# Performance work log

Measured on AMD Instinct MI355X. Metric: run time of the kernel, lower is better.

The kernel has to match this reference:

```python
import jax, jax.numpy as jnp
import numpy as np

B, N, FEAT_DIM = 64, 4096, 256
N_SLOTS, SLOT_DIM, N_ITERS = 6, 64, 3
EPS_LN = 1e-5

def _ln(x, g, b):
    m = jnp.mean(x, axis=-1, keepdims=True)
    v = jnp.mean((x - m) ** 2, axis=-1, keepdims=True)
    return (x - m) * jax.lax.rsqrt(v + EPS_LN) * g + b

def setup_inputs() -> dict:
    key = jax.random.key(0)
    ks = jax.random.split(key, 16)
    def lin(k, out_d, in_d):  # torch Linear default init scale
        bound = 1.0 / np.sqrt(in_d)
        return jax.random.uniform(k, (out_d, in_d), jnp.float32, -bound, bound)
    H = SLOT_DIM
    bound_h = 1.0 / np.sqrt(H)
    return {
        "features": jax.random.normal(ks[0], (B, N, FEAT_DIM), jnp.float32),
        "slot_noise": jax.random.normal(ks[1], (B, N_SLOTS, SLOT_DIM), jnp.float32),
        "slot_mu": jax.random.normal(ks[2], (1, 1, SLOT_DIM), jnp.float32) * 0.02,
        "slot_sigma": jnp.ones((1, 1, SLOT_DIM), jnp.float32) * 0.1,
        "ln_feat_g": jnp.ones((FEAT_DIM,), jnp.float32),
        "ln_feat_b": jnp.zeros((FEAT_DIM,), jnp.float32),
        "ln_slot_g": jnp.ones((SLOT_DIM,), jnp.float32),
        "ln_slot_b": jnp.zeros((SLOT_DIM,), jnp.float32),
        "ln_mlp_g": jnp.ones((SLOT_DIM,), jnp.float32),
        "ln_mlp_b": jnp.zeros((SLOT_DIM,), jnp.float32),
        "Wk": lin(ks[3], SLOT_DIM, FEAT_DIM),
        "Wv": lin(ks[4], SLOT_DIM, FEAT_DIM),
        "Wq": lin(ks[5], SLOT_DIM, SLOT_DIM),
        "W_ih": jax.random.uniform(ks[6], (3 * H, H), jnp.float32, -bound_h, bound_h),
        "W_hh": jax.random.uniform(ks[7], (3 * H, H), jnp.float32, -bound_h, bound_h),
        "b_ih": jax.random.uniform(ks[8], (3 * H,), jnp.float32, -bound_h, bound_h),
        "b_hh": jax.random.uniform(ks[9], (3 * H,), jnp.float32, -bound_h, bound_h),
        "mlp_W1": lin(ks[10], 2 * SLOT_DIM, SLOT_DIM),
        "mlp_b1": jnp.zeros((2 * SLOT_DIM,), jnp.float32),
        "mlp_W2": lin(ks[11], SLOT_DIM, 2 * SLOT_DIM),
        "mlp_b2": jnp.zeros((SLOT_DIM,), jnp.float32),
    }

def _gru(x, h, W_ih, W_hh, b_ih, b_hh):
    # torch.nn.GRUCell semantics; x, h: [M, H]
    gi = x @ W_ih.T + b_ih
    gh = h @ W_hh.T + b_hh
    i_r, i_z, i_n = jnp.split(gi, 3, axis=-1)
    h_r, h_z, h_n = jnp.split(gh, 3, axis=-1)
    r = jax.nn.sigmoid(i_r + h_r)
    z = jax.nn.sigmoid(i_z + h_z)
    n = jnp.tanh(i_n + r * h_n)
    return (1.0 - z) * n + z * h

def reference(features, slot_noise, slot_mu, slot_sigma,
              ln_feat_g, ln_feat_b, ln_slot_g, ln_slot_b, ln_mlp_g, ln_mlp_b,
              Wk, Wv, Wq, W_ih, W_hh, b_ih, b_hh,
              mlp_W1, mlp_b1, mlp_W2, mlp_b2):
    slots = slot_mu + slot_sigma * slot_noise            # [B, K, H]
    f = _ln(features, ln_feat_g, ln_feat_b)              # [B, N, D]
    k = jnp.einsum('bnd,hd->bnh', f, Wk)                 # [B, N, H]
    v = jnp.einsum('bnd,hd->bnh', f, Wv)                 # [B, N, H]
    scale = SLOT_DIM ** (-0.5)
    for _ in range(N_ITERS):
        slots_prev = slots
        s = _ln(slots, ln_slot_g, ln_slot_b)
        q = jnp.einsum('bkh,gh->bkg', s, Wq)             # [B, K, H]
        attn = jnp.einsum('bkh,bnh->bkn', q, k) * scale  # [B, K, N]
        attn = jax.nn.softmax(attn, axis=1)              # softmax over SLOT dim
        attn = attn / (jnp.sum(attn, axis=-1, keepdims=True) + 1e-8)
        updates = jnp.einsum('bkn,bnh->bkh', attn, v)    # [B, K, H]
        h = _gru(updates.reshape(-1, SLOT_DIM), slots_prev.reshape(-1, SLOT_DIM),
                 W_ih, W_hh, b_ih, b_hh)
        slots = h.reshape(B, N_SLOTS, SLOT_DIM)
        m = _ln(slots, ln_mlp_g, ln_mlp_b)
        m = jax.nn.relu(m @ mlp_W1.T + mlp_b1) @ mlp_W2.T + mlp_b2
        slots = slots + m
    return slots
```

## Files before the change

kernel.cpp:

```cpp
#include <hip/hip_runtime.h>
#include <hip/hip_bf16.h>
#include <math.h>

#define B_SZ    64
#define N_TOK   4096
#define D_FEAT  256
#define K_SLOTS 6
#define H_DIM   64
#define N_IT    3
#define CHUNKS  8
#define LNKV_BLOCKS 512
#define TILES_PER_BLOCK 8

typedef __attribute__((ext_vector_type(8))) __bf16 bf16x8;
typedef __attribute__((ext_vector_type(4))) __bf16 bf16x4;
typedef __attribute__((ext_vector_type(4))) float  f32x4v;

__device__ __forceinline__ float wave_reduce_sum(float v) {
    #pragma unroll
    for (int off = 32; off > 0; off >>= 1) v += __shfl_xor(v, off, 64);
    return v;
}
__device__ __forceinline__ float bflo(unsigned u) { return __builtin_bit_cast(float, (unsigned)(u << 16)); }
__device__ __forceinline__ float bfhi(unsigned u) { return __builtin_bit_cast(float, (unsigned)(u & 0xffff0000u)); }

__global__ __launch_bounds__(256) void prep_kernel(
    const float* __restrict__ Wk, const float* __restrict__ Wv,
    const float* __restrict__ noise, const float* __restrict__ mu,
    const float* __restrict__ sigma, const float* __restrict__ Wq,
    const float* __restrict__ W_ih, const float* __restrict__ W_hh,
    const float* __restrict__ W1, const float* __restrict__ W2,
    __bf16* __restrict__ Wfrag, float* __restrict__ slots,
    float* __restrict__ WqT, float* __restrict__ WihT, float* __restrict__ WhhT,
    float* __restrict__ W1T, float* __restrict__ W2T)
{
    const int tg = blockIdx.x * 256 + threadIdx.x;
    if (tg < 4096) {
        const int chunk = tg >> 6, lane = tg & 63;
        const int ct = chunk >> 3, ks = chunk & 7;
        const int outr = ct * 16 + (lane & 15);
        const int dbase = (lane >> 4) * 8 + ks * 32;
        const float* srcw = (outr < 64) ? &Wk[outr * 256] : &Wv[(outr - 64) * 256];
        bf16x8 w8;
        #pragma unroll
        for (int j = 0; j < 8; ++j) w8[j] = (__bf16)srcw[dbase + j];
        *(bf16x8*)&Wfrag[(size_t)tg * 8] = w8;
    } else if (tg < 4096 + 24576) {
        const int i = tg - 4096;
        const int hh = i & 63;
        slots[i] = mu[hh] + sigma[hh] * noise[i];
    } else if (tg < 32768) {
        const int i = tg - 28672;
        WqT[i] = Wq[(i & 63) * 64 + (i >> 6)];
    } else if (tg < 45056) {
        const int i = tg - 32768;
        WihT[i] = W_ih[(i % 192) * 64 + (i / 192)];
    } else if (tg < 57344) {
        const int i = tg - 45056;
        WhhT[i] = W_hh[(i % 192) * 64 + (i / 192)];
    } else if (tg < 65536) {
        const int i = tg - 57344;
        W1T[i] = W1[(i & 127) * 64 + (i >> 7)];
    } else if (tg < 73728) {
        const int i = tg - 65536;
        W2T[i] = W2[(i & 63) * 128 + (i >> 6)];
    }
}

__global__ __launch_bounds__(256, 1) void ln_kv_mfma(
    const float* __restrict__ feat, const float* __restrict__ g,
    const float* __restrict__ bta, const __bf16* __restrict__ Wfrag,
    __bf16* __restrict__ kv)
{
    __shared__ __align__(16) __bf16 W_lds[32768];
    __shared__ __align__(16) __bf16 A_lds[64][264];
    __shared__ __align__(16) __bf16 C_lds[64][136];

    const int t = threadIdx.x;
    const int lane = t & 63;
    const int w = t >> 6;
    const int m15 = lane & 15;
    const int q4 = lane >> 4;

    {
        const uint4* src = (const uint4*)Wfrag;
        uint4* dst = (uint4*)W_lds;
        #pragma unroll
        for (int i = 0; i < 16; ++i) dst[i * 256 + t] = src[i * 256 + t];
    }
    __syncthreads();

    const float4 gg = *(const float4*)&g[lane * 4];
    const float4 bb = *(const float4*)&bta[lane * 4];

    float4 x[16];
    {
        const size_t row0 = (size_t)blockIdx.x * TILES_PER_BLOCK * 64 + w * 16;
        #pragma unroll
        for (int r = 0; r < 16; ++r)
            x[r] = *(const float4*)&feat[(row0 + r) * D_FEAT + lane * 4];
    }

    for (int tile = 0; tile < TILES_PER_BLOCK; ++tile) {
        const size_t tile_row0 = (size_t)blockIdx.x * TILES_PER_BLOCK * 64 + (size_t)tile * 64;

        #pragma unroll
        for (int r = 0; r < 16; ++r) {
            float s1 = x[r].x + x[r].y + x[r].z + x[r].w;
            float s2 = x[r].x * x[r].x + x[r].y * x[r].y + x[r].z * x[r].z + x[r].w * x[r].w;
            s1 = wave_reduce_sum(s1);
            s2 = wave_reduce_sum(s2);
            const float m = s1 * (1.0f / 256.0f);
            const float inv = rsqrtf(s2 * (1.0f / 256.0f) - m * m + 1e-5f);
            bf16x4 y;
            y[0] = (__bf16)((x[r].x - m) * inv * gg.x + bb.x);
            y[1] = (__bf16)((x[r].y - m) * inv * gg.y + bb.y);
            y[2] = (__bf16)((x[r].z - m) * inv * gg.z + bb.z);
            y[3] = (__bf16)((x[r].w - m) * inv * gg.w + bb.w);
            *(bf16x4*)&A_lds[w * 16 + r][lane * 4] = y;
        }

        if (tile + 1 < TILES_PER_BLOCK) {
            const size_t row0 = tile_row0 + 64 + w * 16;
            #pragma unroll
            for (int r = 0; r < 16; ++r)
                x[r] = *(const float4*)&feat[(row0 + r) * D_FEAT + lane * 4];
        }

        bf16x8 af[8];
        #pragma unroll
        for (int ks = 0; ks < 8; ++ks)
            af[ks] = *(const bf16x8*)&A_lds[w * 16 + m15][q4 * 8 + ks * 32];

        f32x4v acc[8];
        #pragma unroll
        for (int ct = 0; ct < 8; ++ct) acc[ct] = (f32x4v){0.f, 0.f, 0.f, 0.f};

        #pragma unroll
        for (int ks = 0; ks < 8; ++ks) {
            #pragma unroll
            for (int ct = 0; ct < 8; ++ct) {
                const bf16x8 bfr = *(const bf16x8*)&W_lds[((ct * 8 + ks) * 64 + lane) * 8];
                acc[ct] = __builtin_amdgcn_mfma_f32_16x16x32_bf16(af[ks], bfr, acc[ct], 0, 0, 0);
            }
        }

        #pragma unroll
        for (int ct = 0; ct < 8; ++ct) {
            #pragma unroll
            for (int reg = 0; reg < 4; ++reg)
                C_lds[w * 16 + q4 * 4 + reg][ct * 16 + m15] = (__bf16)acc[ct][reg];
        }
        const int lr = w * 16 + (lane >> 2);
        const int seg = lane & 3;
        __bf16* dstg = kv + (tile_row0 + lr) * 128 + seg * 32;
        #pragma unroll
        for (int u = 0; u < 4; ++u) {
            const uint4 val = *(const uint4*)&C_lds[lr][seg * 32 + u * 8];
            *(uint4*)&dstg[u * 8] = val;
        }
    }
}

__global__ __launch_bounds__(64) void slot_q0(
    const float* __restrict__ slots, const float* __restrict__ g,
    const float* __restrict__ bta, const float* __restrict__ WqT,
    float* __restrict__ qb)
{
    __shared__ float s_lds[64];
    const int bk = blockIdx.x, h = threadIdx.x;
    const float xv = slots[bk * 64 + h];
    const float s1 = wave_reduce_sum(xv);
    const float s2 = wave_reduce_sum(xv * xv);
    const float m = s1 * (1.0f / 64.0f);
    const float inv = rsqrtf(s2 * (1.0f / 64.0f) - m * m + 1e-5f);
    s_lds[h] = (xv - m) * inv * g[h] + bta[h];
    __syncthreads();
    float acc = 0.f;
    #pragma unroll 8
    for (int j = 0; j < 64; ++j) acc += WqT[j * 64 + h] * s_lds[j];
    qb[bk * 64 + h] = acc;
}

__global__ __launch_bounds__(256) void attn_kernel(
    const float* __restrict__ qb, const __bf16* __restrict__ kv,
    float* __restrict__ U_part, float* __restrict__ S_part)
{
    __shared__ float q_lds[K_SLOTS * 64];
    __shared__ __align__(16) float KVt[64][130];
    __shared__ float p_lds[K_SLOTS][64];
    __shared__ float U_red[4][K_SLOTS][64];
    __shared__ float S_red[4][K_SLOTS];

    const int t = threadIdx.x;
    const int b = blockIdx.y;
    const int chunk = blockIdx.x;
    const int lane = t & 63;
    const int w = t >> 6;
    const int n_loc = t >> 2, sub = t & 3;
    const int h = lane;

    for (int i = t; i < K_SLOTS * 64; i += 256) q_lds[i] = qb[b * K_SLOTS * 64 + i];

    float Uacc[K_SLOTS] = {0, 0, 0, 0, 0, 0};
    float Sacc[K_SLOTS] = {0, 0, 0, 0, 0, 0};

    for (int tile = 0; tile < 8; ++tile) {
        __syncthreads();
        const size_t n0 = (size_t)b * N_TOK + (size_t)chunk * (N_TOK / CHUNKS) + tile * 64;
        {
            const uint4* src = (const uint4*)&kv[(n0 + lane) * 128 + w * 32];
            float2* drow = (float2*)&KVt[lane][w * 32];
            #pragma unroll
            for (int u = 0; u < 4; ++u) {
                const uint4 pk = src[u];
                drow[u * 4 + 0] = make_float2(bflo(pk.x), bfhi(pk.x));
                drow[u * 4 + 1] = make_float2(bflo(pk.y), bfhi(pk.y));
                drow[u * 4 + 2] = make_float2(bflo(pk.z), bfhi(pk.z));
                drow[u * 4 + 3] = make_float2(bflo(pk.w), bfhi(pk.w));
            }
        }
        __syncthreads();

        float part[K_SLOTS] = {0, 0, 0, 0, 0, 0};
        #pragma unroll
        for (int i = 0; i < 16; ++i) {
            const float kvv = KVt[n_loc][sub * 16 + i];
            #pragma unroll
            for (int k = 0; k < K_SLOTS; ++k) part[k] += q_lds[k * 64 + sub * 16 + i] * kvv;
        }
        #pragma unroll
        for (int k = 0; k < K_SLOTS; ++k) {
            part[k] += __shfl_xor(part[k], 1, 64);
            part[k] += __shfl_xor(part[k], 2, 64);
        }
        float mx = part[0];
        #pragma unroll
        for (int k = 1; k < K_SLOTS; ++k) mx = fmaxf(mx, part[k]);
        float e[K_SLOTS], ssum = 0.f;
        #pragma unroll
        for (int k = 0; k < K_SLOTS; ++k) { e[k] = __expf((part[k] - mx) * 0.125f); ssum += e[k]; }
        mx = part[0] * 0.125f;
        #pragma unroll
        for (int k = 1; k < K_SLOTS; ++k) mx = fmaxf(mx, part[k] * 0.125f);
        ssum = 0.f;
        #pragma unroll
        for (int k = 0; k < K_SLOTS; ++k) { e[k] = __expf(part[k] * 0.125f - mx); ssum += e[k]; }
        const float rs = 1.0f / ssum;
        if (sub == 0) {
            #pragma unroll
            for (int k = 0; k < K_SLOTS; ++k) {
                const float p = e[k] * rs;
                p_lds[k][n_loc] = p;
                Sacc[k] += p;
            }
        }
        __syncthreads();

        for (int n = w * 16; n < w * 16 + 16; ++n) {
            const float vv = KVt[n][64 + h];
            #pragma unroll
            for (int k = 0; k < K_SLOTS; ++k) Uacc[k] += p_lds[k][n] * vv;
        }
    }

    #pragma unroll
    for (int k = 0; k < K_SLOTS; ++k) U_red[w][k][h] = Uacc[k];
    #pragma unroll
    for (int k = 0; k < K_SLOTS; ++k) {
        const float s = wave_reduce_sum(Sacc[k]);
        if (lane == 0) S_red[w][k] = s;
    }
    __syncthreads();
    for (int idx = t; idx < K_SLOTS * 64; idx += 256) {
        const int k = idx >> 6, hh = idx & 63;
        const float s = U_red[0][k][hh] + U_red[1][k][hh] + U_red[2][k][hh] + U_red[3][k][hh];
        U_part[(((size_t)b * CHUNKS + chunk) * K_SLOTS + k) * 64 + hh] = s;
    }
    if (t < K_SLOTS) {
        const float s = S_red[0][t] + S_red[1][t] + S_red[2][t] + S_red[3][t];
        S_part[((size_t)b * CHUNKS + chunk) * K_SLOTS + t] = s;
    }
}

__global__ __launch_bounds__(64) void update_kernel(
    const float* __restrict__ U_part, const float* __restrict__ S_part,
    float* __restrict__ slots,
    const float* __restrict__ WihT, const float* __restrict__ WhhT,
    const float* __restrict__ b_ih, const float* __restrict__ b_hh,
    const float* __restrict__ g_mlp, const float* __restrict__ b_mlp,
    const float* __restrict__ W1T, const float* __restrict__ b1,
    const float* __restrict__ W2T, const float* __restrict__ b2,
    const float* __restrict__ g_slot, const float* __restrict__ b_slot,
    const float* __restrict__ WqT, float* __restrict__ qb,
    float* __restrict__ out, int last)
{
    __shared__ float x_lds[64], h_lds[64], m_lds[64], r_lds[128];
    const int bk = blockIdx.x, h = threadIdx.x;
    const int b = bk / K_SLOTS, k = bk % K_SLOTS;

    float Us = 0.f, Ss = 0.f;
    #pragma unroll
    for (int c = 0; c < CHUNKS; ++c)
        Us += U_part[(((size_t)b * CHUNKS + c) * K_SLOTS + k) * 64 + h];
    #pragma unroll
    for (int c = 0; c < CHUNKS; ++c)
        Ss += S_part[((size_t)b * CHUNKS + c) * K_SLOTS + k];

    const float u = Us / (Ss + 1e-8f);
    const float hp = slots[bk * 64 + h];
    x_lds[h] = u;
    h_lds[h] = hp;
    __syncthreads();

    float ir = b_ih[h], iz = b_ih[64 + h], inn = b_ih[128 + h];
    float hr = b_hh[h], hz = b_hh[64 + h], hn = b_hh[128 + h];
    #pragma unroll 4
    for (int j = 0; j < 64; ++j) {
        const float xj = x_lds[j], hj = h_lds[j];
        const float* wi = &WihT[j * 192];
        const float* wh = &WhhT[j * 192];
        ir += wi[h] * xj; iz += wi[64 + h] * xj; inn += wi[128 + h] * xj;
        hr += wh[h] * hj; hz += wh[64 + h] * hj; hn += wh[128 + h] * hj;
    }
    const float r = 1.0f / (1.0f + __expf(-(ir + hr)));
    const float z = 1.0f / (1.0f + __expf(-(iz + hz)));
    const float nn = tanhf(inn + r * hn);
    const float hnew = (1.0f - z) * nn + z * hp;

    const float s1 = wave_reduce_sum(hnew);
    const float s2 = wave_reduce_sum(hnew * hnew);
    const float m = s1 * (1.0f / 64.0f);
    const float inv = rsqrtf(s2 * (1.0f / 64.0f) - m * m + 1e-5f);
    m_lds[h] = (hnew - m) * inv * g_mlp[h] + b_mlp[h];
    __syncthreads();

    float a1 = b1[h], a2 = b1[64 + h];
    #pragma unroll 4
    for (int j = 0; j < 64; ++j) {
        const float mj = m_lds[j];
        a1 += W1T[j * 128 + h] * mj;
        a2 += W1T[j * 128 + 64 + h] * mj;
    }
    r_lds[h] = fmaxf(a1, 0.f);
    r_lds[64 + h] = fmaxf(a2, 0.f);
    __syncthreads();

    float o = b2[h];
    #pragma unroll 4
    for (int c = 0; c < 128; ++c) o += W2T[c * 64 + h] * r_lds[c];

    const float res = hnew + o;
    slots[bk * 64 + h] = res;
    if (last) {
        out[bk * 64 + h] = res;
    } else {
        const float t1 = wave_reduce_sum(res);
        const float t2 = wave_reduce_sum(res * res);
        const float mm = t1 * (1.0f / 64.0f);
        const float ii = rsqrtf(t2 * (1.0f / 64.0f) - mm * mm + 1e-5f);
        m_lds[h] = (res - mm) * ii * g_slot[h] + b_slot[h];
        __syncthreads();
        float qv = 0.f;
        #pragma unroll 8
        for (int j = 0; j < 64; ++j) qv += WqT[j * 64 + h] * m_lds[j];
        qb[bk * 64 + h] = qv;
    }
}

extern "C" void kernel_launch(void* const* d_in, const int* in_sizes, int n_in,
                              void* d_out, int out_size, void* d_ws, size_t ws_size,
                              hipStream_t stream) {
    const float* feat      = (const float*)d_in[0];
    const float* noise     = (const float*)d_in[1];
    const float* mu        = (const float*)d_in[2];
    const float* sigma     = (const float*)d_in[3];
    const float* ln_feat_g = (const float*)d_in[4];
    const float* ln_feat_b = (const float*)d_in[5];
    const float* ln_slot_g = (const float*)d_in[6];
    const float* ln_slot_b = (const float*)d_in[7];
    const float* ln_mlp_g  = (const float*)d_in[8];
    const float* ln_mlp_b  = (const float*)d_in[9];
    const float* Wk        = (const float*)d_in[10];
    const float* Wv        = (const float*)d_in[11];
    const float* Wq        = (const float*)d_in[12];
    const float* W_ih      = (const float*)d_in[13];
    const float* W_hh      = (const float*)d_in[14];
    const float* b_ih      = (const float*)d_in[15];
    const float* b_hh      = (const float*)d_in[16];
    const float* W1        = (const float*)d_in[17];
    const float* b1        = (const float*)d_in[18];
    const float* W2        = (const float*)d_in[19];
    const float* b2        = (const float*)d_in[20];
    float* out = (float*)d_out;

    char* p = (char*)d_ws;
    __bf16* kv    = (__bf16*)p;                 p += (size_t)B_SZ * N_TOK * 128 * 2;
    __bf16* Wfrag = (__bf16*)p;                 p += 32768 * 2;
    float* slots  = (float*)p;                  p += 24576 * 4;
    float* qb     = (float*)p;                  p += 24576 * 4;
    float* U_part = (float*)p;                  p += (size_t)B_SZ * CHUNKS * K_SLOTS * 64 * 4;
    float* S_part = (float*)p;                  p += (size_t)B_SZ * CHUNKS * K_SLOTS * 4;
    float* WqT    = (float*)p;                  p += 4096 * 4;
    float* WihT   = (float*)p;                  p += 12288 * 4;
    float* WhhT   = (float*)p;                  p += 12288 * 4;
    float* W1T    = (float*)p;                  p += 8192 * 4;
    float* W2T    = (float*)p;                  p += 8192 * 4;

    hipLaunchKernelGGL(prep_kernel, dim3(288), dim3(256), 0, stream,
                       Wk, Wv, noise, mu, sigma, Wq, W_ih, W_hh, W1, W2,
                       Wfrag, slots, WqT, WihT, WhhT, W1T, W2T);
    hipLaunchKernelGGL(ln_kv_mfma, dim3(LNKV_BLOCKS), dim3(256), 0, stream,
                       feat, ln_feat_g, ln_feat_b, Wfrag, kv);
    hipLaunchKernelGGL(slot_q0, dim3(384), dim3(64), 0, stream,
                       slots, ln_slot_g, ln_slot_b, WqT, qb);
    for (int it = 0; it < N_IT; ++it) {
        hipLaunchKernelGGL(attn_kernel, dim3(CHUNKS, B_SZ), dim3(256), 0, stream,
                           qb, kv, U_part, S_part);
        hipLaunchKernelGGL(update_kernel, dim3(384), dim3(64), 0, stream,
                           U_part, S_part, slots, WihT, WhhT, b_ih, b_hh,
                           ln_mlp_g, ln_mlp_b, W1T, b1, W2T, b2,
                           ln_slot_g, ln_slot_b, WqT, qb,
                           out, (it == N_IT - 1) ? 1 : 0);
    }
}
```

Before: 575.3 us.

## Fuse all slot iterations into one per-batch kernel with MFMA attention

Replaces the per-iteration attention and update kernel pairs with a single kernel that runs one 1024-thread block per batch. That block computes slot init, q projection, attention with MFMA, GRU and MLP for all three iterations. The LN/KV projection kernel now uses 512-thread blocks and writes K row-major and V transposed so V can be fed directly as MFMA operands. The aim is to remove kernel launches, partial-sum round trips through global memory and fp32 LDS conversion. The cost is that only 64 blocks run the iteration phase, which limits parallelism over a 4096-token sweep per iteration.

```diff
diff --git a/kernel.cpp b/kernel.cpp
--- a/kernel.cpp
+++ b/kernel.cpp
@@ -8,9 +8,8 @@
 #define K_SLOTS 6
 #define H_DIM   64
 #define N_IT    3
-#define CHUNKS  8
-#define LNKV_BLOCKS 512
-#define TILES_PER_BLOCK 8
+#define LNKV_BLOCKS 256
+#define LNKV_TILES  8
 
 typedef __attribute__((ext_vector_type(8))) __bf16 bf16x8;
 typedef __attribute__((ext_vector_type(4))) __bf16 bf16x4;
@@ -21,17 +20,14 @@
     for (int off = 32; off > 0; off >>= 1) v += __shfl_xor(v, off, 64);
     return v;
 }
-__device__ __forceinline__ float bflo(unsigned u) { return __builtin_bit_cast(float, (unsigned)(u << 16)); }
-__device__ __forceinline__ float bfhi(unsigned u) { return __builtin_bit_cast(float, (unsigned)(u & 0xffff0000u)); }
 
 __global__ __launch_bounds__(256) void prep_kernel(
     const float* __restrict__ Wk, const float* __restrict__ Wv,
-    const float* __restrict__ noise, const float* __restrict__ mu,
-    const float* __restrict__ sigma, const float* __restrict__ Wq,
-    const float* __restrict__ W_ih, const float* __restrict__ W_hh,
-    const float* __restrict__ W1, const float* __restrict__ W2,
-    __bf16* __restrict__ Wfrag, float* __restrict__ slots,
-    float* __restrict__ WqT, float* __restrict__ WihT, float* __restrict__ WhhT,
+    const float* __restrict__ Wq, const float* __restrict__ W_ih,
+    const float* __restrict__ W_hh, const float* __restrict__ W1,
+    const float* __restrict__ W2,
+    __bf16* __restrict__ Wfrag, float* __restrict__ WqT,
+    float* __restrict__ WihT, float* __restrict__ WhhT,
     float* __restrict__ W1T, float* __restrict__ W2T)
 {
     const int tg = blockIdx.x * 256 + threadIdx.x;
@@ -45,64 +41,56 @@
         #pragma unroll
         for (int j = 0; j < 8; ++j) w8[j] = (__bf16)srcw[dbase + j];
         *(bf16x8*)&Wfrag[(size_t)tg * 8] = w8;
-    } else if (tg < 4096 + 24576) {
-        const int i = tg - 4096;
-        const int hh = i & 63;
-        slots[i] = mu[hh] + sigma[hh] * noise[i];
+    } else if (tg < 8192) {
+        const int i = tg - 4096;  WqT[i] = Wq[(i & 63) * 64 + (i >> 6)];
+    } else if (tg < 20480) {
+        const int i = tg - 8192;  WihT[i] = W_ih[(i % 192) * 64 + (i / 192)];
     } else if (tg < 32768) {
-        const int i = tg - 28672;
-        WqT[i] = Wq[(i & 63) * 64 + (i >> 6)];
-    } else if (tg < 45056) {
-        const int i = tg - 32768;
-        WihT[i] = W_ih[(i % 192) * 64 + (i / 192)];
-    } else if (tg < 57344) {
-        const int i = tg - 45056;
-        WhhT[i] = W_hh[(i % 192) * 64 + (i / 192)];
-    } else if (tg < 65536) {
-        const int i = tg - 57344;
-        W1T[i] = W1[(i & 127) * 64 + (i >> 7)];
-    } else if (tg < 73728) {
-        const int i = tg - 65536;
-        W2T[i] = W2[(i & 63) * 128 + (i >> 6)];
+        const int i = tg - 20480; WhhT[i] = W_hh[(i % 192) * 64 + (i / 192)];
+    } else if (tg < 40960) {
+        const int i = tg - 32768; W1T[i] = W1[(i & 127) * 64 + (i >> 7)];
+    } else if (tg < 49152) {
+        const int i = tg - 40960; W2T[i] = W2[(i & 63) * 128 + (i >> 6)];
     }
 }
 
-__global__ __launch_bounds__(256, 1) void ln_kv_mfma(
+__global__ __launch_bounds__(512, 2) void ln_kv_mfma(
     const float* __restrict__ feat, const float* __restrict__ g,
     const float* __restrict__ bta, const __bf16* __restrict__ Wfrag,
-    __bf16* __restrict__ kv)
+    __bf16* __restrict__ kbuf, __bf16* __restrict__ vT)
 {
     __shared__ __align__(16) __bf16 W_lds[32768];
-    __shared__ __align__(16) __bf16 A_lds[64][264];
-    __shared__ __align__(16) __bf16 C_lds[64][136];
+    __shared__ __align__(16) __bf16 S_A[8][16 * 272];
 
     const int t = threadIdx.x;
     const int lane = t & 63;
     const int w = t >> 6;
-    const int m15 = lane & 15;
-    const int q4 = lane >> 4;
+    const int m15 = lane & 15, q4 = lane >> 4;
 
     {
         const uint4* src = (const uint4*)Wfrag;
         uint4* dst = (uint4*)W_lds;
         #pragma unroll
-        for (int i = 0; i < 16; ++i) dst[i * 256 + t] = src[i * 256 + t];
+        for (int i = 0; i < 8; ++i) dst[i * 512 + t] = src[i * 512 + t];
     }
     __syncthreads();
 
     const float4 gg = *(const float4*)&g[lane * 4];
     const float4 bb = *(const float4*)&bta[lane * 4];
 
+    const size_t block_row0 = (size_t)blockIdx.x * (LNKV_TILES * 128);
+    const int b  = blockIdx.x >> 2;
+    const int nq = (blockIdx.x & 3) * 1024;
+
+    __bf16* Aw = &S_A[w][0];
+
     float4 x[16];
-    {
-        const size_t row0 = (size_t)blockIdx.x * TILES_PER_BLOCK * 64 + w * 16;
-        #pragma unroll
-        for (int r = 0; r < 16; ++r)
-            x[r] = *(const float4*)&feat[(row0 + r) * D_FEAT + lane * 4];
-    }
-
-    for (int tile = 0; tile < TILES_PER_BLOCK; ++tile) {
-        const size_t tile_row0 = (size_t)blockIdx.x * TILES_PER_BLOCK * 64 + (size_t)tile * 64;
+    #pragma unroll
+    for (int r = 0; r < 16; ++r)
+        x[r] = *(const float4*)&feat[(block_row0 + w * 16 + r) * D_FEAT + lane * 4];
+
+    for (int tile = 0; tile < LNKV_TILES; ++tile) {
+        const size_t trow0 = block_row0 + (size_t)tile * 128;
 
         #pragma unroll
         for (int r = 0; r < 16; ++r) {
@@ -110,32 +98,30 @@
             float s2 = x[r].x * x[r].x + x[r].y * x[r].y + x[r].z * x[r].z + x[r].w * x[r].w;
             s1 = wave_reduce_sum(s1);
             s2 = wave_reduce_sum(s2);
-            const float m = s1 * (1.0f / 256.0f);
-            const float inv = rsqrtf(s2 * (1.0f / 256.0f) - m * m + 1e-5f);
+            const float m = s1 * (1.f / 256.f);
+            const float inv = rsqrtf(s2 * (1.f / 256.f) - m * m + 1e-5f);
             bf16x4 y;
             y[0] = (__bf16)((x[r].x - m) * inv * gg.x + bb.x);
             y[1] = (__bf16)((x[r].y - m) * inv * gg.y + bb.y);
             y[2] = (__bf16)((x[r].z - m) * inv * gg.z + bb.z);
             y[3] = (__bf16)((x[r].w - m) * inv * gg.w + bb.w);
-            *(bf16x4*)&A_lds[w * 16 + r][lane * 4] = y;
-        }
-
-        if (tile + 1 < TILES_PER_BLOCK) {
-            const size_t row0 = tile_row0 + 64 + w * 16;
+            *(bf16x4*)&Aw[r * 272 + lane * 4] = y;
+        }
+
+        if (tile + 1 < LNKV_TILES) {
             #pragma unroll
             for (int r = 0; r < 16; ++r)
-                x[r] = *(const float4*)&feat[(row0 + r) * D_FEAT + lane * 4];
+                x[r] = *(const float4*)&feat[(trow0 + 128 + w * 16 + r) * D_FEAT + lane * 4];
         }
 
         bf16x8 af[8];
         #pragma unroll
         for (int ks = 0; ks < 8; ++ks)
-            af[ks] = *(const bf16x8*)&A_lds[w * 16 + m15][q4 * 8 + ks * 32];
+            af[ks] = *(const bf16x8*)&Aw[m15 * 272 + q4 * 8 + ks * 32];
 
         f32x4v acc[8];
         #pragma unroll
         for (int ct = 0; ct < 8; ++ct) acc[ct] = (f32x4v){0.f, 0.f, 0.f, 0.f};
-
         #pragma unroll
         for (int ks = 0; ks < 8; ++ks) {
             #pragma unroll
@@ -149,222 +135,233 @@
         for (int ct = 0; ct < 8; ++ct) {
             #pragma unroll
             for (int reg = 0; reg < 4; ++reg)
-                C_lds[w * 16 + q4 * 4 + reg][ct * 16 + m15] = (__bf16)acc[ct][reg];
-        }
-        const int lr = w * 16 + (lane >> 2);
-        const int seg = lane & 3;
-        __bf16* dstg = kv + (tile_row0 + lr) * 128 + seg * 32;
-        #pragma unroll
-        for (int u = 0; u < 4; ++u) {
-            const uint4 val = *(const uint4*)&C_lds[lr][seg * 32 + u * 8];
-            *(uint4*)&dstg[u * 8] = val;
+                Aw[(q4 * 4 + reg) * 136 + ct * 16 + m15] = (__bf16)acc[ct][reg];
+        }
+
+        {
+            const int r = lane >> 2, seg = lane & 3;
+            const bf16x8 k0 = *(const bf16x8*)&Aw[r * 136 + seg * 16];
+            const bf16x8 k1 = *(const bf16x8*)&Aw[r * 136 + seg * 16 + 8];
+            __bf16* kd = kbuf + (trow0 + w * 16 + r) * 64 + seg * 16;
+            *(bf16x8*)&kd[0] = k0;
+            *(bf16x8*)&kd[8] = k1;
+        }
+        {
+            bf16x8 v0, v1;
+            #pragma unroll
+            for (int i = 0; i < 8; ++i) v0[i] = Aw[i * 136 + 64 + lane];
+            #pragma unroll
+            for (int i = 0; i < 8; ++i) v1[i] = Aw[(8 + i) * 136 + 64 + lane];
+            __bf16* vd = vT + ((size_t)b * 64 + lane) * N_TOK + nq + tile * 128 + w * 16;
+            *(bf16x8*)&vd[0] = v0;
+            *(bf16x8*)&vd[8] = v1;
         }
     }
 }
 
-__global__ __launch_bounds__(64) void slot_q0(
-    const float* __restrict__ slots, const float* __restrict__ g,
-    const float* __restrict__ bta, const float* __restrict__ WqT,
-    float* __restrict__ qb)
+__global__ __launch_bounds__(1024, 4) void iters_kernel(
+    const __bf16* __restrict__ kbuf, const __bf16* __restrict__ vT,
+    const float* __restrict__ noise, const float* __restrict__ mu,
+    const float* __restrict__ sigma,
+    const float* __restrict__ g_slot, const float* __restrict__ b_slot,
+    const float* __restrict__ g_mlp, const float* __restrict__ b_mlp,
+    const float* __restrict__ WqT,
+    const float* __restrict__ WihT, const float* __restrict__ WhhT,
+    const float* __restrict__ b_ih, const float* __restrict__ b_hh,
+    const float* __restrict__ W1T, const float* __restrict__ b1,
+    const float* __restrict__ W2T, const float* __restrict__ b2,
+    float* __restrict__ out)
 {
-    __shared__ float s_lds[64];
-    const int bk = blockIdx.x, h = threadIdx.x;
-    const float xv = slots[bk * 64 + h];
-    const float s1 = wave_reduce_sum(xv);
-    const float s2 = wave_reduce_sum(xv * xv);
-    const float m = s1 * (1.0f / 64.0f);
-    const float inv = rsqrtf(s2 * (1.0f / 64.0f) - m * m + 1e-5f);
-    s_lds[h] = (xv - m) * inv * g[h] + bta[h];
-    __syncthreads();
-    float acc = 0.f;
-    #pragma unroll 8
-    for (int j = 0; j < 64; ++j) acc += WqT[j * 64 + h] * s_lds[j];
-    qb[bk * 64 + h] = acc;
-}
-
-__global__ __launch_bounds__(256) void attn_kernel(
-    const float* __restrict__ qb, const __bf16* __restrict__ kv,
-    float* __restrict__ U_part, float* __restrict__ S_part)
-{
-    __shared__ float q_lds[K_SLOTS * 64];
-    __shared__ __align__(16) float KVt[64][130];
-    __shared__ float p_lds[K_SLOTS][64];
-    __shared__ float U_red[4][K_SLOTS][64];
-    __shared__ float S_red[4][K_SLOTS];
-
-    const int t = threadIdx.x;
-    const int b = blockIdx.y;
-    const int chunk = blockIdx.x;
-    const int lane = t & 63;
-    const int w = t >> 6;
-    const int n_loc = t >> 2, sub = t & 3;
-    const int h = lane;
-
-    for (int i = t; i < K_SLOTS * 64; i += 256) q_lds[i] = qb[b * K_SLOTS * 64 + i];
-
-    float Uacc[K_SLOTS] = {0, 0, 0, 0, 0, 0};
-    float Sacc[K_SLOTS] = {0, 0, 0, 0, 0, 0};
-
-    for (int tile = 0; tile < 8; ++tile) {
-        __syncthreads();
-        const size_t n0 = (size_t)b * N_TOK + (size_t)chunk * (N_TOK / CHUNKS) + tile * 64;
-        {
-            const uint4* src = (const uint4*)&kv[(n0 + lane) * 128 + w * 32];
-            float2* drow = (float2*)&KVt[lane][w * 32];
-            #pragma unroll
-            for (int u = 0; u < 4; ++u) {
-                const uint4 pk = src[u];
-                drow[u * 4 + 0] = make_float2(bflo(pk.x), bfhi(pk.x));
-                drow[u * 4 + 1] = make_float2(bflo(pk.y), bfhi(pk.y));
-                drow[u * 4 + 2] = make_float2(bflo(pk.z), bfhi(pk.z));
-                drow[u * 4 + 3] = make_float2(bflo(pk.w), bfhi(pk.w));
-            }
-        }
-        __syncthreads();
-
-        float part[K_SLOTS] = {0, 0, 0, 0, 0, 0};
-        #pragma unroll
-        for (int i = 0; i < 16; ++i) {
-            const float kvv = KVt[n_loc][sub * 16 + i];
-            #pragma unroll
-            for (int k = 0; k < K_SLOTS; ++k) part[k] += q_lds[k * 64 + sub * 16 + i] * kvv;
-        }
-        #pragma unroll
-        for (int k = 0; k < K_SLOTS; ++k) {
-            part[k] += __shfl_xor(part[k], 1, 64);
-            part[k] += __shfl_xor(part[k], 2, 64);
-        }
-        float mx = part[0];
-        #pragma unroll
-        for (int k = 1; k < K_SLOTS; ++k) mx = fmaxf(mx, part[k]);
-        float e[K_SLOTS], ssum = 0.f;
-        #pragma unroll
-        for (int k = 0; k < K_SLOTS; ++k) { e[k] = __expf((part[k] - mx) * 0.125f); ssum += e[k]; }
-        mx = part[0] * 0.125f;
-        #pragma unroll
-        for (int k = 1; k < K_SLOTS; ++k) mx = fmaxf(mx, part[k] * 0.125f);
-        ssum = 0.f;
-        #pragma unroll
-        for (int k = 0; k < K_SLOTS; ++k) { e[k] = __expf(part[k] * 0.125f - mx); ssum += e[k]; }
-        const float rs = 1.0f / ssum;
-        if (sub == 0) {
-            #pragma unroll
-            for (int k = 0; k < K_SLOTS; ++k) {
-                const float p = e[k] * rs;
-                p_lds[k][n_loc] = p;
-                Sacc[k] += p;
-            }
-        }
-        __syncthreads();
-
-        for (int n = w * 16; n < w * 16 + 16; ++n) {
-            const float vv = KVt[n][64 + h];
-            #pragma unroll
-            for (int k = 0; k < K_SLOTS; ++k) Uacc[k] += p_lds[k][n] * vv;
-        }
-    }
-
-    #pragma unroll
-    for (int k = 0; k < K_SLOTS; ++k) U_red[w][k][h] = Uacc[k];
-    #pragma unroll
-    for (int k = 0; k < K_SLOTS; ++k) {
-        const float s = wave_reduce_sum(Sacc[k]);
-        if (lane == 0) S_red[w][k] = s;
+    __shared__ float q_lds[16][64];
+    __shared__ __align__(16) __bf16 p_lds[16][8 * 264];
+    __shared__ float U_red[16][6][64];
+    __shared__ float S_red[16][6][16];
+    __shared__ float slots_lds[6][64], x_lds[6][64], m_lds[6][64], s_lds[6][64];
+    __shared__ float gi_lds[1152], gh_lds[1152];
+    __shared__ float r_lds[6][128];
+    __shared__ float S2[6][16];
+
+    const int t = threadIdx.x, lane = t & 63, w = t >> 6;
+    const int m15 = lane & 15, q4 = lane >> 4;
+    const int b = blockIdx.x;
+    const int kk = t >> 6, hh = t & 63;
+
+    for (int i = lane; i < 528; i += 64) p_lds[w][6 * 264 + i] = (__bf16)0.f;
+    if (t >= 384) { const int i = t - 384; q_lds[6 + (i >> 6)][i & 63] = 0.f; }
+
+    if (t < 384) {
+        const float sv = mu[hh] + sigma[hh] * noise[(b * K_SLOTS + kk) * 64 + hh];
+        slots_lds[kk][hh] = sv;
+        const float s1 = wave_reduce_sum(sv), s2 = wave_reduce_sum(sv * sv);
+        const float m = s1 * (1.f / 64.f);
+        const float inv = rsqrtf(s2 * (1.f / 64.f) - m * m + 1e-5f);
+        s_lds[kk][hh] = (sv - m) * inv * g_slot[hh] + b_slot[hh];
+        float qv = 0.f;
+        #pragma unroll 8
+        for (int j = 0; j < 64; ++j) qv += WqT[j * 64 + hh] * s_lds[kk][j];
+        q_lds[kk][hh] = qv;
     }
     __syncthreads();
-    for (int idx = t; idx < K_SLOTS * 64; idx += 256) {
-        const int k = idx >> 6, hh = idx & 63;
-        const float s = U_red[0][k][hh] + U_red[1][k][hh] + U_red[2][k][hh] + U_red[3][k][hh];
-        U_part[(((size_t)b * CHUNKS + chunk) * K_SLOTS + k) * 64 + hh] = s;
-    }
-    if (t < K_SLOTS) {
-        const float s = S_red[0][t] + S_red[1][t] + S_red[2][t] + S_red[3][t];
-        S_part[((size_t)b * CHUNKS + chunk) * K_SLOTS + t] = s;
-    }
-}
-
-__global__ __launch_bounds__(64) void update_kernel(
-    const float* __restrict__ U_part, const float* __restrict__ S_part,
-    float* __restrict__ slots,
-    const float* __restrict__ WihT, const float* __restrict__ WhhT,
-    const float* __restrict__ b_ih, const float* __restrict__ b_hh,
-    const float* __restrict__ g_mlp, const float* __restrict__ b_mlp,
-    const float* __restrict__ W1T, const float* __restrict__ b1,
-    const float* __restrict__ W2T, const float* __restrict__ b2,
-    const float* __restrict__ g_slot, const float* __restrict__ b_slot,
-    const float* __restrict__ WqT, float* __restrict__ qb,
-    float* __restrict__ out, int last)
-{
-    __shared__ float x_lds[64], h_lds[64], m_lds[64], r_lds[128];
-    const int bk = blockIdx.x, h = threadIdx.x;
-    const int b = bk / K_SLOTS, k = bk % K_SLOTS;
-
-    float Us = 0.f, Ss = 0.f;
-    #pragma unroll
-    for (int c = 0; c < CHUNKS; ++c)
-        Us += U_part[(((size_t)b * CHUNKS + c) * K_SLOTS + k) * 64 + h];
-    #pragma unroll
-    for (int c = 0; c < CHUNKS; ++c)
-        Ss += S_part[((size_t)b * CHUNKS + c) * K_SLOTS + k];
-
-    const float u = Us / (Ss + 1e-8f);
-    const float hp = slots[bk * 64 + h];
-    x_lds[h] = u;
-    h_lds[h] = hp;
-    __syncthreads();
-
-    float ir = b_ih[h], iz = b_ih[64 + h], inn = b_ih[128 + h];
-    float hr = b_hh[h], hz = b_hh[64 + h], hn = b_hh[128 + h];
-    #pragma unroll 4
-    for (int j = 0; j < 64; ++j) {
-        const float xj = x_lds[j], hj = h_lds[j];
-        const float* wi = &WihT[j * 192];
-        const float* wh = &WhhT[j * 192];
-        ir += wi[h] * xj; iz += wi[64 + h] * xj; inn += wi[128 + h] * xj;
-        hr += wh[h] * hj; hz += wh[64 + h] * hj; hn += wh[128 + h] * hj;
-    }
-    const float r = 1.0f / (1.0f + __expf(-(ir + hr)));
-    const float z = 1.0f / (1.0f + __expf(-(iz + hz)));
-    const float nn = tanhf(inn + r * hn);
-    const float hnew = (1.0f - z) * nn + z * hp;
-
-    const float s1 = wave_reduce_sum(hnew);
-    const float s2 = wave_reduce_sum(hnew * hnew);
-    const float m = s1 * (1.0f / 64.0f);
-    const float inv = rsqrtf(s2 * (1.0f / 64.0f) - m * m + 1e-5f);
-    m_lds[h] = (hnew - m) * inv * g_mlp[h] + b_mlp[h];
-    __syncthreads();
-
-    float a1 = b1[h], a2 = b1[64 + h];
-    #pragma unroll 4
-    for (int j = 0; j < 64; ++j) {
-        const float mj = m_lds[j];
-        a1 += W1T[j * 128 + h] * mj;
-        a2 += W1T[j * 128 + 64 + h] * mj;
-    }
-    r_lds[h] = fmaxf(a1, 0.f);
-    r_lds[64 + h] = fmaxf(a2, 0.f);
-    __syncthreads();
-
-    float o = b2[h];
-    #pragma unroll 4
-    for (int c = 0; c < 128; ++c) o += W2T[c * 64 + h] * r_lds[c];
-
-    const float res = hnew + o;
-    slots[bk * 64 + h] = res;
-    if (last) {
-        out[bk * 64 + h] = res;
-    } else {
-        const float t1 = wave_reduce_sum(res);
-        const float t2 = wave_reduce_sum(res * res);
-        const float mm = t1 * (1.0f / 64.0f);
-        const float ii = rsqrtf(t2 * (1.0f / 64.0f) - mm * mm + 1e-5f);
-        m_lds[h] = (res - mm) * ii * g_slot[h] + b_slot[h];
-        __syncthreads();
-        float qv = 0.f;
-        #pragma unroll 8
-        for (int j = 0; j < 64; ++j) qv += WqT[j * 64 + h] * m_lds[j];
-        qb[bk * 64 + h] = qv;
+
+    for (int iter = 0; iter < N_IT; ++iter) {
+        bf16x8 qf0, qf1;
+        #pragma unroll
+        for (int j = 0; j < 8; ++j) qf0[j] = (__bf16)q_lds[m15][q4 * 8 + j];
+        #pragma unroll
+        for (int j = 0; j < 8; ++j) qf1[j] = (__bf16)q_lds[m15][q4 * 8 + 32 + j];
+
+        const __bf16* kb = kbuf + ((size_t)b * N_TOK + w * 256) * 64;
+        float Sacc[6] = {0.f, 0.f, 0.f, 0.f, 0.f, 0.f};
+        #pragma unroll 2
+        for (int gi = 0; gi < 16; ++gi) {
+            const bf16x8 k0 = *(const bf16x8*)&kb[(gi * 16 + m15) * 64 + q4 * 8];
+            const bf16x8 k1 = *(const bf16x8*)&kb[(gi * 16 + m15) * 64 + q4 * 8 + 32];
+            f32x4v a = (f32x4v){0.f, 0.f, 0.f, 0.f};
+            a = __builtin_amdgcn_mfma_f32_16x16x32_bf16(qf0, k0, a, 0, 0, 0);
+            a = __builtin_amdgcn_mfma_f32_16x16x32_bf16(qf1, k1, a, 0, 0, 0);
+            const float l4 = __shfl(a[0], m15 + 16, 64);
+            const float l5 = __shfl(a[1], m15 + 16, 64);
+            if (q4 == 0) {
+                float l[6] = {a[0] * 0.125f, a[1] * 0.125f, a[2] * 0.125f,
+                              a[3] * 0.125f, l4 * 0.125f, l5 * 0.125f};
+                float mx = l[0];
+                #pragma unroll
+                for (int k = 1; k < 6; ++k) mx = fmaxf(mx, l[k]);
+                float e[6], ss = 0.f;
+                #pragma unroll
+                for (int k = 0; k < 6; ++k) { e[k] = __expf(l[k] - mx); ss += e[k]; }
+                const float rs = 1.f / ss;
+                const int tok = gi * 16 + m15;
+                #pragma unroll
+                for (int k = 0; k < 6; ++k) {
+                    const float p = e[k] * rs;
+                    p_lds[w][k * 264 + tok] = (__bf16)p;
+                    Sacc[k] += p;
+                }
+            }
+        }
+
+        f32x4v U[4];
+        #pragma unroll
+        for (int ct = 0; ct < 4; ++ct) U[ct] = (f32x4v){0.f, 0.f, 0.f, 0.f};
+        #pragma unroll
+        for (int kc = 0; kc < 4; ++kc) {
+            const bf16x8 pa0 = *(const bf16x8*)&p_lds[w][(m15 & 7) * 264 + kc * 64 + q4 * 8];
+            const bf16x8 pa1 = *(const bf16x8*)&p_lds[w][(m15 & 7) * 264 + kc * 64 + q4 * 8 + 32];
+            #pragma unroll
+            for (int ct = 0; ct < 4; ++ct) {
+                const __bf16* vb = vT + ((size_t)b * 64 + ct * 16 + m15) * N_TOK
+                                      + w * 256 + kc * 64 + q4 * 8;
+                const bf16x8 v0 = *(const bf16x8*)&vb[0];
+                const bf16x8 v1 = *(const bf16x8*)&vb[32];
+                U[ct] = __builtin_amdgcn_mfma_f32_16x16x32_bf16(pa0, v0, U[ct], 0, 0, 0);
+                U[ct] = __builtin_amdgcn_mfma_f32_16x16x32_bf16(pa1, v1, U[ct], 0, 0, 0);
+            }
+        }
+
+        #pragma unroll
+        for (int ct = 0; ct < 4; ++ct) {
+            #pragma unroll
+            for (int reg = 0; reg < 4; ++reg) {
+                const int row = q4 * 4 + reg;
+                if (row < 6) U_red[w][row][ct * 16 + m15] = U[ct][reg];
+            }
+        }
+        if (q4 == 0) {
+            #pragma unroll
+            for (int k = 0; k < 6; ++k) S_red[w][k][m15] = Sacc[k];
+        }
+        __syncthreads();
+
+        float U_tot = 0.f;
+        if (t < 384) {
+            #pragma unroll
+            for (int w16 = 0; w16 < 16; ++w16) U_tot += U_red[w16][kk][hh];
+        }
+        if (t < 96) {
+            const int k2 = t >> 4, m2 = t & 15;
+            float s = 0.f;
+            #pragma unroll
+            for (int w16 = 0; w16 < 16; ++w16) s += S_red[w16][k2][m2];
+            S2[k2][m2] = s;
+        }
+        __syncthreads();
+        if (t < 384) {
+            float St = 0.f;
+            #pragma unroll
+            for (int m2 = 0; m2 < 16; ++m2) St += S2[kk][m2];
+            x_lds[kk][hh] = U_tot / (St + 1e-8f);
+        }
+        __syncthreads();
+
+        for (int idx = t; idx < 1152; idx += 1024) {
+            const int kq = idx / 192, r = idx % 192;
+            float gi = b_ih[r], gh = b_hh[r];
+            #pragma unroll 4
+            for (int j4 = 0; j4 < 16; ++j4) {
+                const float4 xx = *(const float4*)&x_lds[kq][j4 * 4];
+                const float4 hv = *(const float4*)&slots_lds[kq][j4 * 4];
+                gi += xx.x * WihT[(j4 * 4 + 0) * 192 + r] + xx.y * WihT[(j4 * 4 + 1) * 192 + r]
+                    + xx.z * WihT[(j4 * 4 + 2) * 192 + r] + xx.w * WihT[(j4 * 4 + 3) * 192 + r];
+                gh += hv.x * WhhT[(j4 * 4 + 0) * 192 + r] + hv.y * WhhT[(j4 * 4 + 1) * 192 + r]
+                    + hv.z * WhhT[(j4 * 4 + 2) * 192 + r] + hv.w * WhhT[(j4 * 4 + 3) * 192 + r];
+            }
+            gi_lds[idx] = gi;
+            gh_lds[idx] = gh;
+        }
+        __syncthreads();
+
+        float hnew = 0.f;
+        if (t < 384) {
+            const int base = kk * 192;
+            const float rg = 1.f / (1.f + __expf(-(gi_lds[base + hh] + gh_lds[base + hh])));
+            const float zg = 1.f / (1.f + __expf(-(gi_lds[base + 64 + hh] + gh_lds[base + 64 + hh])));
+            const float ng = tanhf(gi_lds[base + 128 + hh] + rg * gh_lds[base + 128 + hh]);
+            hnew = (1.f - zg) * ng + zg * slots_lds[kk][hh];
+            const float s1 = wave_reduce_sum(hnew), s2 = wave_reduce_sum(hnew * hnew);
+            const float m = s1 * (1.f / 64.f);
+            const float inv = rsqrtf(s2 * (1.f / 64.f) - m * m + 1e-5f);
+            m_lds[kk][hh] = (hnew - m) * inv * g_mlp[hh] + b_mlp[hh];
+        }
+        __syncthreads();
+
+        if (t < 768) {
+            const int k3 = t >> 7, c = t & 127;
+            float a = b1[c];
+            #pragma unroll 4
+            for (int j4 = 0; j4 < 16; ++j4) {
+                const float4 mm = *(const float4*)&m_lds[k3][j4 * 4];
+                a += mm.x * W1T[(j4 * 4 + 0) * 128 + c] + mm.y * W1T[(j4 * 4 + 1) * 128 + c]
+                   + mm.z * W1T[(j4 * 4 + 2) * 128 + c] + mm.w * W1T[(j4 * 4 + 3) * 128 + c];
+            }
+            r_lds[k3][c] = fmaxf(a, 0.f);
+        }
+        __syncthreads();
+
+        if (t < 384) {
+            float o = b2[hh];
+            #pragma unroll 4
+            for (int c4 = 0; c4 < 32; ++c4) {
+                const float4 rr = *(const float4*)&r_lds[kk][c4 * 4];
+                o += rr.x * W2T[(c4 * 4 + 0) * 64 + hh] + rr.y * W2T[(c4 * 4 + 1) * 64 + hh]
+                   + rr.z * W2T[(c4 * 4 + 2) * 64 + hh] + rr.w * W2T[(c4 * 4 + 3) * 64 + hh];
+            }
+            const float res = hnew + o;
+            slots_lds[kk][hh] = res;
+            if (iter == N_IT - 1) {
+                out[(b * K_SLOTS + kk) * 64 + hh] = res;
+            } else {
+                const float s1 = wave_reduce_sum(res), s2 = wave_reduce_sum(res * res);
+                const float m = s1 * (1.f / 64.f);
+                const float inv = rsqrtf(s2 * (1.f / 64.f) - m * m + 1e-5f);
+                s_lds[kk][hh] = (res - m) * inv * g_slot[hh] + b_slot[hh];
+                float qv = 0.f;
+                #pragma unroll 8
+                for (int j = 0; j < 64; ++j) qv += WqT[j * 64 + hh] * s_lds[kk][j];
+                q_lds[kk][hh] = qv;
+            }
+        }
+        __syncthreads();
     }
 }
 
@@ -395,32 +392,22 @@
     float* out = (float*)d_out;
 
     char* p = (char*)d_ws;
-    __bf16* kv    = (__bf16*)p;                 p += (size_t)B_SZ * N_TOK * 128 * 2;
-    __bf16* Wfrag = (__bf16*)p;                 p += 32768 * 2;
-    float* slots  = (float*)p;                  p += 24576 * 4;
-    float* qb     = (float*)p;                  p += 24576 * 4;
-    float* U_part = (float*)p;                  p += (size_t)B_SZ * CHUNKS * K_SLOTS * 64 * 4;
-    float* S_part = (float*)p;                  p += (size_t)B_SZ * CHUNKS * K_SLOTS * 4;
-    float* WqT    = (float*)p;                  p += 4096 * 4;
-    float* WihT   = (float*)p;                  p += 12288 * 4;
-    float* WhhT   = (float*)p;                  p += 12288 * 4;
-    float* W1T    = (float*)p;                  p += 8192 * 4;
-    float* W2T    = (float*)p;                  p += 8192 * 4;
-
-    hipLaunchKernelGGL(prep_kernel, dim3(288), dim3(256), 0, stream,
-                       Wk, Wv, noise, mu, sigma, Wq, W_ih, W_hh, W1, W2,
-                       Wfrag, slots, WqT, WihT, WhhT, W1T, W2T);
-    hipLaunchKernelGGL(ln_kv_mfma, dim3(LNKV_BLOCKS), dim3(256), 0, stream,
-                       feat, ln_feat_g, ln_feat_b, Wfrag, kv);
-    hipLaunchKernelGGL(slot_q0, dim3(384), dim3(64), 0, stream,
-                       slots, ln_slot_g, ln_slot_b, WqT, qb);
-    for (int it = 0; it < N_IT; ++it) {
-        hipLaunchKernelGGL(attn_kernel, dim3(CHUNKS, B_SZ), dim3(256), 0, stream,
-                           qb, kv, U_part, S_part);
-        hipLaunchKernelGGL(update_kernel, dim3(384), dim3(64), 0, stream,
-                           U_part, S_part, slots, WihT, WhhT, b_ih, b_hh,
-                           ln_mlp_g, ln_mlp_b, W1T, b1, W2T, b2,
-                           ln_slot_g, ln_slot_b, WqT, qb,
-                           out, (it == N_IT - 1) ? 1 : 0);
-    }
+    __bf16* kbuf  = (__bf16*)p;  p += (size_t)B_SZ * N_TOK * 64 * 2;
+    __bf16* vTb   = (__bf16*)p;  p += (size_t)B_SZ * 64 * N_TOK * 2;
+    __bf16* Wfrag = (__bf16*)p;  p += 32768 * 2;
+    float* WqT    = (float*)p;   p += 4096 * 4;
+    float* WihT   = (float*)p;   p += 12288 * 4;
+    float* WhhT   = (float*)p;   p += 12288 * 4;
+    float* W1T    = (float*)p;   p += 8192 * 4;
+    float* W2T    = (float*)p;   p += 8192 * 4;
+
+    hipLaunchKernelGGL(prep_kernel, dim3(192), dim3(256), 0, stream,
+                       Wk, Wv, Wq, W_ih, W_hh, W1, W2,
+                       Wfrag, WqT, WihT, WhhT, W1T, W2T);
+    hipLaunchKernelGGL(ln_kv_mfma, dim3(LNKV_BLOCKS), dim3(512), 0, stream,
+                       feat, ln_feat_g, ln_feat_b, Wfrag, kbuf, vTb);
+    hipLaunchKernelGGL(iters_kernel, dim3(B_SZ), dim3(1024), 0, stream,
+                       kbuf, vTb, noise, mu, sigma,
+                       ln_slot_g, ln_slot_b, ln_mlp_g, ln_mlp_b,
+                       WqT, WihT, WhhT, b_ih, b_hh, W1T, b1, W2T, b2, out);
 }
```

Result: slower. 695.1 us (+20.8%).
